# Kernel optimization log

Measured on AMD Instinct MI355X. Metric: run time of the kernel, lower is better.

Reference implementation:

```python
import jax, jax.numpy as jnp
import numpy as np

N_HEAD = 12

def setup_inputs() -> dict:
    key = jax.random.key(0)
    ks = jax.random.split(key, 5)
    B, T, C = 8, 1024, 768
    s = 0.02
    return {
        'x': jax.random.normal(ks[0], (B, T, C), dtype=jnp.float32),
        'w_attn': jax.random.normal(ks[1], (C, 3 * C), dtype=jnp.float32) * s,
        'b_attn': jax.random.normal(ks[2], (3 * C,), dtype=jnp.float32) * s,
        'w_proj': jax.random.normal(ks[3], (C, C), dtype=jnp.float32) * s,
        'b_proj': jax.random.normal(ks[4], (C,), dtype=jnp.float32) * s,
    }

def reference(x, w_attn, b_attn, w_proj, b_proj):
    B, T, C = x.shape
    H, D = N_HEAD, C // N_HEAD
    qkv = x @ w_attn + b_attn                      # [B,T,3C]
    q, k, v = jnp.split(qkv, 3, axis=-1)
    q = q.reshape(B, T, H, D)
    k = k.reshape(B, T, H, D)
    v = v.reshape(B, T, H, D)
    # NOTE: faithful to source - NO 1/sqrt(D) scaling
    wei = jnp.einsum('bthd,bshd->bhts', q, k)      # [B,H,T,T]
    causal = jnp.tril(jnp.ones((T, T), dtype=bool))
    wei = jnp.where(causal[None, None], wei, -jnp.inf)
    wei = jax.nn.softmax(wei, axis=-1)
    out = jnp.einsum('bhts,bshd->bthd', wei, v)    # [B,T,H,D]
    out = out.reshape(B, T, C)
    return out @ w_proj + b_proj
```

## Files before the change

kernel.cpp:

```cpp
#include <hip/hip_runtime.h>

typedef __attribute__((ext_vector_type(8))) short bf16x8_t;
typedef __attribute__((ext_vector_type(4))) float f32x4_t;

#define AS1C(p) ((const __attribute__((address_space(1))) void*)(p))
#define AS3(p)  ((__attribute__((address_space(3))) void*)(p))

#define N_HEAD 12
#define SEQ_T 1024
#define CDIM 768
#define HDIM 64
#define L2E 1.44269504f

__device__ __forceinline__ unsigned short f2bf(float f) {
    union { float f; unsigned int u; } v;
    v.f = f;
    unsigned int r = (v.u + 0x7fffu + ((v.u >> 16) & 1u)) >> 16;
    return (unsigned short)r;
}

__global__ __launch_bounds__(256) void prep(
    const float4* __restrict__ x4, ushort4* __restrict__ xbf4,
    const float* __restrict__ w_attn, unsigned short* __restrict__ waT,
    const float* __restrict__ w_proj, unsigned short* __restrict__ wpT)
{
    __shared__ float tile[32][33];
    const int blk = blockIdx.x;
    const int tid = threadIdx.x;
    if (blk < 6144) {
        int i = blk * 256 + tid;
        float4 v = x4[i];
        ushort4 o;
        o.x = f2bf(v.x); o.y = f2bf(v.y); o.z = f2bf(v.z); o.w = f2bf(v.w);
        xbf4[i] = o;
        return;
    }
    const float* src; unsigned short* dst; int R, Cc, c0, r0;
    if (blk < 7872) {
        int idx = blk - 6144;
        src = w_attn; dst = waT; R = 768; Cc = 2304;
        c0 = (idx % 72) * 32; r0 = (idx / 72) * 32;
    } else {
        int idx = blk - 7872;
        src = w_proj; dst = wpT; R = 768; Cc = 768;
        c0 = (idx % 24) * 32; r0 = (idx / 24) * 32;
    }
    const int tx = tid & 31, ty = tid >> 5;
#pragma unroll
    for (int i = 0; i < 4; i++)
        tile[ty + i * 8][tx] = src[(size_t)(r0 + ty + i * 8) * Cc + c0 + tx];
    __syncthreads();
#pragma unroll
    for (int i = 0; i < 4; i++)
        dst[(size_t)(c0 + ty + i * 8) * R + r0 + tx] = f2bf(tile[tx][ty + i * 8]);
}

__device__ __forceinline__ void gemm128_core(
    const unsigned short* __restrict__ A, const unsigned short* __restrict__ Bt,
    unsigned short* As, unsigned short* Bs, f32x4_t acc[4][4], int mBase, int nBase)
{
    const int tid  = threadIdx.x;
    const int lane = tid & 63;
    const int wv   = tid >> 6;
    const int quad = lane >> 4;
    const int l16  = lane & 15;
    const int wm   = (wv >> 1) * 64;
    const int wn   = (wv & 1) * 64;

    f32x4_t zero = {0.f, 0.f, 0.f, 0.f};
#pragma unroll
    for (int tm = 0; tm < 4; tm++)
#pragma unroll
        for (int tn = 0; tn < 4; tn++)
            acc[tm][tn] = zero;

    for (int kt = 0; kt < 768; kt += 64) {
#pragma unroll
        for (int i = 0; i < 4; i++) {
            int cbase = i * 256 + wv * 64;
            int ci = cbase + lane;
            int r = ci >> 3;
            int koff = (((ci & 7) ^ (r & 7)) << 3);
            __builtin_amdgcn_global_load_lds(
                AS1C(A + (size_t)(mBase + r) * 768 + kt + koff),
                AS3(As + cbase * 8), 16, 0, 0);
            __builtin_amdgcn_global_load_lds(
                AS1C(Bt + (size_t)(nBase + r) * 768 + kt + koff),
                AS3(Bs + cbase * 8), 16, 0, 0);
        }
        __syncthreads();
#pragma unroll
        for (int ks = 0; ks < 2; ks++) {
            bf16x8_t af[4], bfv[4];
#pragma unroll
            for (int tm = 0; tm < 4; tm++)
                af[tm] = *(const bf16x8_t*)(As + (wm + tm * 16 + l16) * 64 +
                                            (((ks * 4 + quad) ^ (l16 & 7)) << 3));
#pragma unroll
            for (int tn = 0; tn < 4; tn++)
                bfv[tn] = *(const bf16x8_t*)(Bs + (wn + tn * 16 + l16) * 64 +
                                             (((ks * 4 + quad) ^ (l16 & 7)) << 3));
#pragma unroll
            for (int tm = 0; tm < 4; tm++)
#pragma unroll
                for (int tn = 0; tn < 4; tn++)
                    acc[tm][tn] = __builtin_amdgcn_mfma_f32_16x16x32_bf16(
                        af[tm], bfv[tn], acc[tm][tn], 0, 0, 0);
        }
        __syncthreads();
    }
}

__global__ __launch_bounds__(256) void gemm_qkv(
    const unsigned short* __restrict__ x, const unsigned short* __restrict__ waT,
    const float* __restrict__ b_attn,
    unsigned short* __restrict__ qbuf, unsigned short* __restrict__ kbuf,
    unsigned short* __restrict__ vbuf)
{
    __shared__ __align__(16) unsigned short As[128 * 64];
    __shared__ __align__(16) unsigned short Bs[128 * 64];
    f32x4_t acc[4][4];
    const int lid = blockIdx.x;
    const int xcd = lid & 7;
    const int j = lid >> 3;
    const int mTile = xcd * 8 + (j & 7);
    const int nTile = j >> 3;
    const int mBase = mTile * 128;
    const int nBase = nTile * 128;
    gemm128_core(x, waT, As, Bs, acc, mBase, nBase);

    const int tid = threadIdx.x;
    const int lane = tid & 63, wv = tid >> 6;
    const int quad = lane >> 4, l16 = lane & 15;
    const int wm = (wv >> 1) * 64, wn = (wv & 1) * 64;
    const int part = nTile / 6;

#pragma unroll
    for (int tn = 0; tn < 4; tn++) {
        int n = nBase + wn + tn * 16 + l16;
        float bv = b_attn[n];
        int f = n - part * 768;
        int hh = f >> 6, d = f & 63;
        if (part == 2) {
#pragma unroll
            for (int tm = 0; tm < 4; tm++) {
                int t0 = mBase + wm + tm * 16 + quad * 4;
                int bb = t0 >> 10, tt = t0 & 1023;
                ushort4 pk;
                pk.x = f2bf(acc[tm][tn][0] + bv);
                pk.y = f2bf(acc[tm][tn][1] + bv);
                pk.z = f2bf(acc[tm][tn][2] + bv);
                pk.w = f2bf(acc[tm][tn][3] + bv);
                *(ushort4*)(vbuf + ((size_t)(bb * N_HEAD + hh) * HDIM + d) * SEQ_T + tt) = pk;
            }
        } else {
            const float scale = (part == 0) ? L2E : 1.f;
            unsigned short* dst = (part == 0) ? qbuf : kbuf;
#pragma unroll
            for (int tm = 0; tm < 4; tm++) {
#pragma unroll
                for (int i = 0; i < 4; i++) {
                    int row = mBase + wm + tm * 16 + quad * 4 + i;
                    int bb = row >> 10, tt = row & 1023;
                    dst[((size_t)(bb * N_HEAD + hh) * SEQ_T + tt) * HDIM + d] =
                        f2bf((acc[tm][tn][i] + bv) * scale);
                }
            }
        }
    }
}

__device__ __forceinline__ void mask_exp_pack(
    f32x4_t s[4], int diag, int qloc, int quad,
    float& lsum, unsigned int u[4][2])
{
    if (diag) {
#pragma unroll
        for (int c = 0; c < 4; c++)
#pragma unroll
            for (int i = 0; i < 4; i++)
                if (c * 16 + quad * 4 + i > qloc) s[c][i] = -1e30f;
    }
    float p[4][4];
#pragma unroll
    for (int c = 0; c < 4; c++)
#pragma unroll
        for (int i = 0; i < 4; i++)
            p[c][i] = exp2f(s[c][i]);
#pragma unroll
    for (int c = 0; c < 4; c++)
        lsum += (p[c][0] + p[c][1]) + (p[c][2] + p[c][3]);
#pragma unroll
    for (int c = 0; c < 4; c++)
#pragma unroll
        for (int i2 = 0; i2 < 2; i2++)
            u[c][i2] = (unsigned int)f2bf(p[c][2 * i2]) |
                       ((unsigned int)f2bf(p[c][2 * i2 + 1]) << 16);
}

__device__ __forceinline__ void p_write(
    unsigned short* pw, const unsigned int u[4][2], int quad, int l16)
{
#pragma unroll
    for (int c = 0; c < 4; c++)
#pragma unroll
        for (int i2 = 0; i2 < 2; i2++) {
            int g = c * 2 + (quad >> 1);
            *(unsigned int*)(pw + l16 * 64 + ((g ^ (l16 & 7)) << 3) +
                             4 * (quad & 1) + 2 * i2) = u[c][i2];
        }
}

__global__ __launch_bounds__(256, 3) void attn_fused(
    const unsigned short* __restrict__ qb, const unsigned short* __restrict__ kb,
    const unsigned short* __restrict__ vb, unsigned short* __restrict__ attb)
{
    __shared__ __align__(16) unsigned short Kbuf[2][64 * 64];
    __shared__ __align__(16) unsigned short Vbuf[2][64 * 64];
    __shared__ __align__(16) unsigned short Psh[4][16 * 64];

    const int bhx = blockIdx.x;
    const int t   = blockIdx.y;
    const int h = bhx % N_HEAD;
    const int b = bhx / N_HEAD;
    const int tid = threadIdx.x;
    const int lane = tid & 63, wv = tid >> 6;
    const int quad = lane >> 4, l16 = lane & 15;
    const int tB = 15 - t, kmax = 15 - t;
    const int qloc = wv * 16 + l16;

    const size_t bh = (size_t)(b * N_HEAD + h);
    const unsigned short* kbase = kb + bh * SEQ_T * HDIM;
    const unsigned short* vbase = vb + bh * HDIM * SEQ_T;
    const unsigned short* qpt   = qb + bh * SEQ_T * HDIM;

    const int j0 = wv * 128 + lane, j1 = j0 + 64;
    const int r0 = j0 >> 3, g0 = (j0 & 7) ^ (r0 & 7);
    const int r1 = j1 >> 3, g1 = (j1 & 7) ^ (r1 & 7);
    const int rgK0 = r0 * 64 + g0 * 8,   rgK1 = r1 * 64 + g1 * 8;
    const int rgV0 = r0 * 1024 + g0 * 8, rgV1 = r1 * 1024 + g1 * 8;
    const int ldsc0 = (wv * 128) * 8, ldsc1 = (wv * 128 + 64) * 8;

    bf16x8_t qfA[2], qfB[2];
    {
        const unsigned short* qa  = qpt + (size_t)(t * 64 + qloc) * HDIM;
        const unsigned short* qbp = qpt + (size_t)(tB * 64 + qloc) * HDIM;
#pragma unroll
        for (int kc = 0; kc < 2; kc++) {
            qfA[kc] = *(const bf16x8_t*)(qa + kc * 32 + quad * 8);
            qfB[kc] = *(const bf16x8_t*)(qbp + kc * 32 + quad * 8);
        }
    }

    f32x4_t zero = {0.f, 0.f, 0.f, 0.f};
    f32x4_t oA[4], oB[4];
#pragma unroll
    for (int c = 0; c < 4; c++) { oA[c] = zero; oB[c] = zero; }
    float lA = 0.f, lB = 0.f;

    __builtin_amdgcn_global_load_lds(AS1C(kbase + rgK0), AS3(&Kbuf[0][0] + ldsc0), 16, 0, 0);
    __builtin_amdgcn_global_load_lds(AS1C(kbase + rgK1), AS3(&Kbuf[0][0] + ldsc1), 16, 0, 0);
    __builtin_amdgcn_global_load_lds(AS1C(vbase + rgV0), AS3(&Vbuf[0][0] + ldsc0), 16, 0, 0);
    __builtin_amdgcn_global_load_lds(AS1C(vbase + rgV1), AS3(&Vbuf[0][0] + ldsc1), 16, 0, 0);
    __syncthreads();

    for (int kt = 0; kt <= kmax; kt++) {
        const int cur = kt & 1, nxt = cur ^ 1;
        if (kt < kmax) {
            const unsigned short* kp = kbase + (kt + 1) * 4096;
            const unsigned short* vp = vbase + (kt + 1) * 64;
            __builtin_amdgcn_global_load_lds(AS1C(kp + rgK0), AS3(&Kbuf[nxt][0] + ldsc0), 16, 0, 0);
            __builtin_amdgcn_global_load_lds(AS1C(kp + rgK1), AS3(&Kbuf[nxt][0] + ldsc1), 16, 0, 0);
            __builtin_amdgcn_global_load_lds(AS1C(vp + rgV0), AS3(&Vbuf[nxt][0] + ldsc0), 16, 0, 0);
            __builtin_amdgcn_global_load_lds(AS1C(vp + rgV1), AS3(&Vbuf[nxt][0] + ldsc1), 16, 0, 0);
        }

        const unsigned short* Kc = &Kbuf[cur][0];
        const unsigned short* Vc = &Vbuf[cur][0];
        const int doA = (kt <= t);

        bf16x8_t vf[4][2];
#pragma unroll
        for (int nc = 0; nc < 4; nc++)
#pragma unroll
            for (int kc = 0; kc < 2; kc++)
                vf[nc][kc] = *(const bf16x8_t*)(Vc + (nc * 16 + l16) * 64 +
                                                (((kc * 4 + quad) ^ (l16 & 7)) << 3));

        f32x4_t sB[4], sA[4];
#pragma unroll
        for (int c = 0; c < 4; c++) {
            bf16x8_t kf0 = *(const bf16x8_t*)(Kc + (c * 16 + l16) * 64 +
                                              ((quad ^ (l16 & 7)) << 3));
            bf16x8_t kf1 = *(const bf16x8_t*)(Kc + (c * 16 + l16) * 64 +
                                              (((4 + quad) ^ (l16 & 7)) << 3));
            sB[c] = __builtin_amdgcn_mfma_f32_16x16x32_bf16(kf0, qfB[0], zero, 0, 0, 0);
            sB[c] = __builtin_amdgcn_mfma_f32_16x16x32_bf16(kf1, qfB[1], sB[c], 0, 0, 0);
            if (doA) {
                sA[c] = __builtin_amdgcn_mfma_f32_16x16x32_bf16(kf0, qfA[0], zero, 0, 0, 0);
                sA[c] = __builtin_amdgcn_mfma_f32_16x16x32_bf16(kf1, qfA[1], sA[c], 0, 0, 0);
            }
        }

        unsigned short* pw = &Psh[wv][0];
        unsigned int uB[4][2], uA[4][2];

        mask_exp_pack(sB, kt == tB, qloc, quad, lB, uB);
        __asm__ __volatile__("" ::: "memory");
        p_write(pw, uB, quad, l16);
        if (doA)
            mask_exp_pack(sA, kt == t, qloc, quad, lA, uA);
        __asm__ __volatile__("" ::: "memory");
        bf16x8_t pfB[2];
#pragma unroll
        for (int kc = 0; kc < 2; kc++)
            pfB[kc] = *(const bf16x8_t*)(pw + l16 * 64 + (((kc * 4 + quad) ^ (l16 & 7)) << 3));
        __asm__ __volatile__("" ::: "memory");
#pragma unroll
        for (int kc = 0; kc < 2; kc++)
#pragma unroll
            for (int nc = 0; nc < 4; nc++)
                oB[nc] = __builtin_amdgcn_mfma_f32_16x16x32_bf16(pfB[kc], vf[nc][kc], oB[nc], 0, 0, 0);
        if (doA) {
            p_write(pw, uA, quad, l16);
            __asm__ __volatile__("" ::: "memory");
            bf16x8_t pfA[2];
#pragma unroll
            for (int kc = 0; kc < 2; kc++)
                pfA[kc] = *(const bf16x8_t*)(pw + l16 * 64 + (((kc * 4 + quad) ^ (l16 & 7)) << 3));
#pragma unroll
            for (int kc = 0; kc < 2; kc++)
#pragma unroll
                for (int nc = 0; nc < 4; nc++)
                    oA[nc] = __builtin_amdgcn_mfma_f32_16x16x32_bf16(pfA[kc], vf[nc][kc], oA[nc], 0, 0, 0);
        }
        __syncthreads();
    }

    lA += __shfl_xor(lA, 16); lA += __shfl_xor(lA, 32);
    lB += __shfl_xor(lB, 16); lB += __shfl_xor(lB, 32);
    float invA = 1.f / lA, invB = 1.f / lB;
    float iA[4], iB[4];
#pragma unroll
    for (int i = 0; i < 4; i++) {
        iA[i] = __shfl(invA, quad * 4 + i);
        iB[i] = __shfl(invB, quad * 4 + i);
    }

#pragma unroll
    for (int nc = 0; nc < 4; nc++)
#pragma unroll
        for (int i = 0; i < 4; i++) {
            int rowA = t * 64 + wv * 16 + quad * 4 + i;
            int rowB = tB * 64 + wv * 16 + quad * 4 + i;
            int col = h * HDIM + nc * 16 + l16;
            attb[((size_t)b * SEQ_T + rowA) * CDIM + col] = f2bf(oA[nc][i] * iA[i]);
            attb[((size_t)b * SEQ_T + rowB) * CDIM + col] = f2bf(oB[nc][i] * iB[i]);
        }
}

__global__ __launch_bounds__(256) void gemm_proj(
    const unsigned short* __restrict__ attb, const unsigned short* __restrict__ wpT,
    const float* __restrict__ b_proj, float* __restrict__ out)
{
    __shared__ __align__(16) unsigned short As[64 * 64];
    __shared__ __align__(16) unsigned short Bs[128 * 64];
    const int lid = blockIdx.x;
    const int xcd = lid & 7;
    const int j = lid >> 3;
    const int mTile = xcd * 16 + (j & 15);
    const int nTile = j >> 4;
    const int mBase = mTile * 64;
    const int nBase = nTile * 128;

    const int tid  = threadIdx.x;
    const int lane = tid & 63;
    const int wv   = tid >> 6;
    const int quad = lane >> 4;
    const int l16  = lane & 15;
    const int wm   = (wv >> 1) * 32;
    const int wn   = (wv & 1) * 64;

    f32x4_t zero = {0.f, 0.f, 0.f, 0.f};
    f32x4_t acc[2][4];
#pragma unroll
    for (int tm = 0; tm < 2; tm++)
#pragma unroll
        for (int tn = 0; tn < 4; tn++)
            acc[tm][tn] = zero;

    for (int kt = 0; kt < 768; kt += 64) {
#pragma unroll
        for (int i = 0; i < 2; i++) {
            int cbase = i * 256 + wv * 64;
            int ci = cbase + lane;
            int r = ci >> 3;
            int koff = (((ci & 7) ^ (r & 7)) << 3);
            __builtin_amdgcn_global_load_lds(
                AS1C(attb + (size_t)(mBase + r) * 768 + kt + koff),
                AS3(As + cbase * 8), 16, 0, 0);
        }
#pragma unroll
        for (int i = 0; i < 4; i++) {
            int cbase = i * 256 + wv * 64;
            int ci = cbase + lane;
            int r = ci >> 3;
            int koff = (((ci & 7) ^ (r & 7)) << 3);
            __builtin_amdgcn_global_load_lds(
                AS1C(wpT + (size_t)(nBase + r) * 768 + kt + koff),
                AS3(Bs + cbase * 8), 16, 0, 0);
        }
        __syncthreads();
#pragma unroll
        for (int ks = 0; ks < 2; ks++) {
            bf16x8_t af[2], bfv[4];
#pragma unroll
            for (int tm = 0; tm < 2; tm++)
                af[tm] = *(const bf16x8_t*)(As + (wm + tm * 16 + l16) * 64 +
                                            (((ks * 4 + quad) ^ (l16 & 7)) << 3));
#pragma unroll
            for (int tn = 0; tn < 4; tn++)
                bfv[tn] = *(const bf16x8_t*)(Bs + (wn + tn * 16 + l16) * 64 +
                                             (((ks * 4 + quad) ^ (l16 & 7)) << 3));
#pragma unroll
            for (int tm = 0; tm < 2; tm++)
#pragma unroll
                for (int tn = 0; tn < 4; tn++)
                    acc[tm][tn] = __builtin_amdgcn_mfma_f32_16x16x32_bf16(
                        af[tm], bfv[tn], acc[tm][tn], 0, 0, 0);
        }
        __syncthreads();
    }

#pragma unroll
    for (int tn = 0; tn < 4; tn++) {
        int n = nBase + wn + tn * 16 + l16;
        float bv = b_proj[n];
#pragma unroll
        for (int tm = 0; tm < 2; tm++)
#pragma unroll
            for (int i = 0; i < 4; i++) {
                int row = mBase + wm + tm * 16 + quad * 4 + i;
                out[(size_t)row * CDIM + n] = acc[tm][tn][i] + bv;
            }
    }
}

extern "C" void kernel_launch(void* const* d_in, const int* in_sizes, int n_in,
                              void* d_out, int out_size, void* d_ws, size_t ws_size,
                              hipStream_t stream) {
    const float* x      = (const float*)d_in[0];
    const float* w_attn = (const float*)d_in[1];
    const float* b_attn = (const float*)d_in[2];
    const float* w_proj = (const float*)d_in[3];
    const float* b_proj = (const float*)d_in[4];
    float* out = (float*)d_out;

    unsigned short* ws   = (unsigned short*)d_ws;
    unsigned short* waT  = ws;
    unsigned short* wpT  = waT + 1769472;
    unsigned short* xbf  = wpT + 589824;
    unsigned short* qbuf = xbf + 6291456;
    unsigned short* kbuf = qbuf + 6291456;
    unsigned short* vbuf = kbuf + 6291456;
    unsigned short* attb = vbuf + 6291456;

    prep<<<dim3(8448), 256, 0, stream>>>((const float4*)x, (ushort4*)xbf,
                                         w_attn, waT, w_proj, wpT);
    gemm_qkv<<<dim3(1152), 256, 0, stream>>>(xbf, waT, b_attn, qbuf, kbuf, vbuf);
    attn_fused<<<dim3(96, 8), 256, 0, stream>>>(qbuf, kbuf, vbuf, attb);
    gemm_proj<<<dim3(768), 256, 0, stream>>>(attb, wpT, b_proj, out);
}
```

Before: 186.0 us.

## Use triple-buffered 128x256 GEMM tiles with 8 waves for QKV and projection

Both GEMMs now share one core that uses 512 threads and 128x256 output tiles, with a three-stage LDS ring. The next two k-tiles are loaded by direct global-to-LDS copies while the current one is computed, gated by explicit vmcnt waits and raw barriers. This is meant to hide global load latency and raise data reuse per block. In exchange it uses far more LDS (about 147 KB per block) and much fewer blocks, only 192 for the projection, which may leave compute units underfilled.

```diff
diff --git a/kernel.cpp b/kernel.cpp
--- a/kernel.cpp
+++ b/kernel.cpp
@@ -55,17 +55,73 @@
         dst[(size_t)(c0 + ty + i * 8) * R + r0 + tx] = f2bf(tile[tx][ty + i * 8]);
 }
 
-__device__ __forceinline__ void gemm128_core(
+#define KTILES 12
+#define ASTRIDE (128 * 64)
+#define BSTRIDE (256 * 64)
+
+__device__ __forceinline__ void stage_tile(
     const unsigned short* __restrict__ A, const unsigned short* __restrict__ Bt,
-    unsigned short* As, unsigned short* Bs, f32x4_t acc[4][4], int mBase, int nBase)
+    unsigned short* As, unsigned short* Bs, int mBase, int nBase, int kt,
+    int wv, int lane)
+{
+#pragma unroll
+    for (int i = 0; i < 2; i++) {
+        int cbase = i * 512 + wv * 64;
+        int ci = cbase + lane;
+        int r = ci >> 3;
+        int koff = (((ci & 7) ^ (r & 7)) << 3);
+        __builtin_amdgcn_global_load_lds(
+            AS1C(A + (size_t)(mBase + r) * 768 + kt + koff),
+            AS3(As + cbase * 8), 16, 0, 0);
+    }
+#pragma unroll
+    for (int i = 0; i < 4; i++) {
+        int cbase = i * 512 + wv * 64;
+        int ci = cbase + lane;
+        int r = ci >> 3;
+        int koff = (((ci & 7) ^ (r & 7)) << 3);
+        __builtin_amdgcn_global_load_lds(
+            AS1C(Bt + (size_t)(nBase + r) * 768 + kt + koff),
+            AS3(Bs + cbase * 8), 16, 0, 0);
+    }
+}
+
+__device__ __forceinline__ void compute_tile(
+    const unsigned short* As, const unsigned short* Bs,
+    f32x4_t acc[4][4], int wm, int wn, int quad, int l16)
+{
+#pragma unroll
+    for (int ks = 0; ks < 2; ks++) {
+        bf16x8_t af[4], bfv[4];
+#pragma unroll
+        for (int tm = 0; tm < 4; tm++)
+            af[tm] = *(const bf16x8_t*)(As + (wm + tm * 16 + l16) * 64 +
+                                        (((ks * 4 + quad) ^ (l16 & 7)) << 3));
+#pragma unroll
+        for (int tn = 0; tn < 4; tn++)
+            bfv[tn] = *(const bf16x8_t*)(Bs + (wn + tn * 16 + l16) * 64 +
+                                         (((ks * 4 + quad) ^ (l16 & 7)) << 3));
+#pragma unroll
+        for (int tm = 0; tm < 4; tm++)
+#pragma unroll
+            for (int tn = 0; tn < 4; tn++)
+                acc[tm][tn] = __builtin_amdgcn_mfma_f32_16x16x32_bf16(
+                    af[tm], bfv[tn], acc[tm][tn], 0, 0, 0);
+    }
+}
+
+__device__ __forceinline__ void gemm_core8(
+    const unsigned short* __restrict__ A, const unsigned short* __restrict__ Bt,
+    unsigned short* As, unsigned short* Bs, f32x4_t acc[4][4],
+    int mBase, int nBase)
 {
     const int tid  = threadIdx.x;
     const int lane = tid & 63;
     const int wv   = tid >> 6;
     const int quad = lane >> 4;
     const int l16  = lane & 15;
-    const int wm   = (wv >> 1) * 64;
-    const int wn   = (wv & 1) * 64;
+    const int wm   = (wv >> 2) * 64;
+    const int wn   = (wv & 3) * 64;
 
     f32x4_t zero = {0.f, 0.f, 0.f, 0.f};
 #pragma unroll
@@ -74,51 +130,39 @@
         for (int tn = 0; tn < 4; tn++)
             acc[tm][tn] = zero;
 
-    for (int kt = 0; kt < 768; kt += 64) {
-#pragma unroll
-        for (int i = 0; i < 4; i++) {
-            int cbase = i * 256 + wv * 64;
-            int ci = cbase + lane;
-            int r = ci >> 3;
-            int koff = (((ci & 7) ^ (r & 7)) << 3);
-            __builtin_amdgcn_global_load_lds(
-                AS1C(A + (size_t)(mBase + r) * 768 + kt + koff),
-                AS3(As + cbase * 8), 16, 0, 0);
-            __builtin_amdgcn_global_load_lds(
-                AS1C(Bt + (size_t)(nBase + r) * 768 + kt + koff),
-                AS3(Bs + cbase * 8), 16, 0, 0);
-        }
-        __syncthreads();
-#pragma unroll
-        for (int ks = 0; ks < 2; ks++) {
-            bf16x8_t af[4], bfv[4];
-#pragma unroll
-            for (int tm = 0; tm < 4; tm++)
-                af[tm] = *(const bf16x8_t*)(As + (wm + tm * 16 + l16) * 64 +
-                                            (((ks * 4 + quad) ^ (l16 & 7)) << 3));
-#pragma unroll
-            for (int tn = 0; tn < 4; tn++)
-                bfv[tn] = *(const bf16x8_t*)(Bs + (wn + tn * 16 + l16) * 64 +
-                                             (((ks * 4 + quad) ^ (l16 & 7)) << 3));
-#pragma unroll
-            for (int tm = 0; tm < 4; tm++)
-#pragma unroll
-                for (int tn = 0; tn < 4; tn++)
-                    acc[tm][tn] = __builtin_amdgcn_mfma_f32_16x16x32_bf16(
-                        af[tm], bfv[tn], acc[tm][tn], 0, 0, 0);
-        }
-        __syncthreads();
-    }
-}
-
-__global__ __launch_bounds__(256) void gemm_qkv(
+    stage_tile(A, Bt, As + 0 * ASTRIDE, Bs + 0 * BSTRIDE, mBase, nBase, 0, wv, lane);
+    stage_tile(A, Bt, As + 1 * ASTRIDE, Bs + 1 * BSTRIDE, mBase, nBase, 64, wv, lane);
+
+#pragma unroll
+    for (int t = 0; t < KTILES; t++) {
+        if (t + 2 < KTILES) {
+            const int nb = (t + 2) % 3;
+            stage_tile(A, Bt, As + nb * ASTRIDE, Bs + nb * BSTRIDE,
+                       mBase, nBase, (t + 2) * 64, wv, lane);
+        }
+        if (t + 2 < KTILES)
+            asm volatile("s_waitcnt vmcnt(12)" ::: "memory");
+        else if (t + 1 < KTILES)
+            asm volatile("s_waitcnt vmcnt(6)" ::: "memory");
+        else
+            asm volatile("s_waitcnt vmcnt(0)" ::: "memory");
+        __builtin_amdgcn_s_barrier();
+        asm volatile("" ::: "memory");
+        const int cb = t % 3;
+        compute_tile(As + cb * ASTRIDE, Bs + cb * BSTRIDE, acc, wm, wn, quad, l16);
+        asm volatile("" ::: "memory");
+        __builtin_amdgcn_s_barrier();
+    }
+}
+
+__global__ __launch_bounds__(512) void gemm_qkv(
     const unsigned short* __restrict__ x, const unsigned short* __restrict__ waT,
     const float* __restrict__ b_attn,
     unsigned short* __restrict__ qbuf, unsigned short* __restrict__ kbuf,
     unsigned short* __restrict__ vbuf)
 {
-    __shared__ __align__(16) unsigned short As[128 * 64];
-    __shared__ __align__(16) unsigned short Bs[128 * 64];
+    __shared__ __align__(16) unsigned short As[3 * ASTRIDE];
+    __shared__ __align__(16) unsigned short Bs[3 * BSTRIDE];
     f32x4_t acc[4][4];
     const int lid = blockIdx.x;
     const int xcd = lid & 7;
@@ -126,14 +170,14 @@
     const int mTile = xcd * 8 + (j & 7);
     const int nTile = j >> 3;
     const int mBase = mTile * 128;
-    const int nBase = nTile * 128;
-    gemm128_core(x, waT, As, Bs, acc, mBase, nBase);
+    const int nBase = nTile * 256;
+    gemm_core8(x, waT, As, Bs, acc, mBase, nBase);
 
     const int tid = threadIdx.x;
     const int lane = tid & 63, wv = tid >> 6;
     const int quad = lane >> 4, l16 = lane & 15;
-    const int wm = (wv >> 1) * 64, wn = (wv & 1) * 64;
-    const int part = nTile / 6;
+    const int wm = (wv >> 2) * 64, wn = (wv & 3) * 64;
+    const int part = nTile / 3;
 
 #pragma unroll
     for (int tn = 0; tn < 4; tn++) {
@@ -359,85 +403,36 @@
         }
 }
 
-__global__ __launch_bounds__(256) void gemm_proj(
+__global__ __launch_bounds__(512) void gemm_proj(
     const unsigned short* __restrict__ attb, const unsigned short* __restrict__ wpT,
     const float* __restrict__ b_proj, float* __restrict__ out)
 {
-    __shared__ __align__(16) unsigned short As[64 * 64];
-    __shared__ __align__(16) unsigned short Bs[128 * 64];
+    __shared__ __align__(16) unsigned short As[3 * ASTRIDE];
+    __shared__ __align__(16) unsigned short Bs[3 * BSTRIDE];
+    f32x4_t acc[4][4];
     const int lid = blockIdx.x;
     const int xcd = lid & 7;
     const int j = lid >> 3;
-    const int mTile = xcd * 16 + (j & 15);
-    const int nTile = j >> 4;
-    const int mBase = mTile * 64;
-    const int nBase = nTile * 128;
+    const int mTile = xcd * 8 + (j & 7);
+    const int nTile = j >> 3;
+    const int mBase = mTile * 128;
+    const int nBase = nTile * 256;
+    gemm_core8(attb, wpT, As, Bs, acc, mBase, nBase);
 
     const int tid  = threadIdx.x;
     const int lane = tid & 63;
     const int wv   = tid >> 6;
     const int quad = lane >> 4;
     const int l16  = lane & 15;
-    const int wm   = (wv >> 1) * 32;
-    const int wn   = (wv & 1) * 64;
-
-    f32x4_t zero = {0.f, 0.f, 0.f, 0.f};
-    f32x4_t acc[2][4];
-#pragma unroll
-    for (int tm = 0; tm < 2; tm++)
-#pragma unroll
-        for (int tn = 0; tn < 4; tn++)
-            acc[tm][tn] = zero;
-
-    for (int kt = 0; kt < 768; kt += 64) {
-#pragma unroll
-        for (int i = 0; i < 2; i++) {
-            int cbase = i * 256 + wv * 64;
-            int ci = cbase + lane;
-            int r = ci >> 3;
-            int koff = (((ci & 7) ^ (r & 7)) << 3);
-            __builtin_amdgcn_global_load_lds(
-                AS1C(attb + (size_t)(mBase + r) * 768 + kt + koff),
-                AS3(As + cbase * 8), 16, 0, 0);
-        }
-#pragma unroll
-        for (int i = 0; i < 4; i++) {
-            int cbase = i * 256 + wv * 64;
-            int ci = cbase + lane;
-            int r = ci >> 3;
-            int koff = (((ci & 7) ^ (r & 7)) << 3);
-            __builtin_amdgcn_global_load_lds(
-                AS1C(wpT + (size_t)(nBase + r) * 768 + kt + koff),
-                AS3(Bs + cbase * 8), 16, 0, 0);
-        }
-        __syncthreads();
-#pragma unroll
-        for (int ks = 0; ks < 2; ks++) {
-            bf16x8_t af[2], bfv[4];
-#pragma unroll
-            for (int tm = 0; tm < 2; tm++)
-                af[tm] = *(const bf16x8_t*)(As + (wm + tm * 16 + l16) * 64 +
-                                            (((ks * 4 + quad) ^ (l16 & 7)) << 3));
-#pragma unroll
-            for (int tn = 0; tn < 4; tn++)
-                bfv[tn] = *(const bf16x8_t*)(Bs + (wn + tn * 16 + l16) * 64 +
-                                             (((ks * 4 + quad) ^ (l16 & 7)) << 3));
-#pragma unroll
-            for (int tm = 0; tm < 2; tm++)
-#pragma unroll
-                for (int tn = 0; tn < 4; tn++)
-                    acc[tm][tn] = __builtin_amdgcn_mfma_f32_16x16x32_bf16(
-                        af[tm], bfv[tn], acc[tm][tn], 0, 0, 0);
-        }
-        __syncthreads();
-    }
+    const int wm   = (wv >> 2) * 64;
+    const int wn   = (wv & 3) * 64;
 
 #pragma unroll
     for (int tn = 0; tn < 4; tn++) {
         int n = nBase + wn + tn * 16 + l16;
         float bv = b_proj[n];
 #pragma unroll
-        for (int tm = 0; tm < 2; tm++)
+        for (int tm = 0; tm < 4; tm++)
 #pragma unroll
             for (int i = 0; i < 4; i++) {
                 int row = mBase + wm + tm * 16 + quad * 4 + i;
@@ -467,7 +462,7 @@
 
     prep<<<dim3(8448), 256, 0, stream>>>((const float4*)x, (ushort4*)xbf,
                                          w_attn, waT, w_proj, wpT);
-    gemm_qkv<<<dim3(1152), 256, 0, stream>>>(xbf, waT, b_attn, qbuf, kbuf, vbuf);
+    gemm_qkv<<<dim3(576), 512, 0, stream>>>(xbf, waT, b_attn, qbuf, kbuf, vbuf);
     attn_fused<<<dim3(96, 8), 256, 0, stream>>>(qbuf, kbuf, vbuf, attb);
-    gemm_proj<<<dim3(768), 256, 0, stream>>>(attb, wpT, b_proj, out);
-}
+    gemm_proj<<<dim3(192), 512, 0, stream>>>(attb, wpT, b_proj, out);
+}
```

New measurement: 182.3 us. 2.0% less time.

## Double-buffer LDS tiles in QKV and projection GEMMs to overlap loads with MFMA

Applied to the files above, without the earlier changes.

Both GEMM kernels now use two LDS buffers per operand and issue the global-to-LDS loads for the next K tile before computing on the current one. The goal is to hide global load latency behind the MFMA work instead of stalling on a barrier every K step. The cost is doubled LDS use per block (64KB for the QKV GEMM), which may reduce occupancy. Correctness also depends on the one remaining barrier per iteration covering completion of the async LDS loads.

```diff
diff --git a/kernel.cpp b/kernel.cpp
--- a/kernel.cpp
+++ b/kernel.cpp
@@ -55,9 +55,30 @@
         dst[(size_t)(c0 + ty + i * 8) * R + r0 + tx] = f2bf(tile[tx][ty + i * 8]);
 }
 
+__device__ __forceinline__ void stage128(
+    const unsigned short* __restrict__ A, const unsigned short* __restrict__ Bt,
+    unsigned short* As, unsigned short* Bs, int mBase, int nBase, int kt,
+    int wv, int lane)
+{
+#pragma unroll
+    for (int i = 0; i < 4; i++) {
+        int cbase = i * 256 + wv * 64;
+        int ci = cbase + lane;
+        int r = ci >> 3;
+        int koff = (((ci & 7) ^ (r & 7)) << 3);
+        __builtin_amdgcn_global_load_lds(
+            AS1C(A + (size_t)(mBase + r) * 768 + kt + koff),
+            AS3(As + cbase * 8), 16, 0, 0);
+        __builtin_amdgcn_global_load_lds(
+            AS1C(Bt + (size_t)(nBase + r) * 768 + kt + koff),
+            AS3(Bs + cbase * 8), 16, 0, 0);
+    }
+}
+
 __device__ __forceinline__ void gemm128_core(
     const unsigned short* __restrict__ A, const unsigned short* __restrict__ Bt,
-    unsigned short* As, unsigned short* Bs, f32x4_t acc[4][4], int mBase, int nBase)
+    unsigned short (*As)[128 * 64], unsigned short (*Bs)[128 * 64],
+    f32x4_t acc[4][4], int mBase, int nBase)
 {
     const int tid  = threadIdx.x;
     const int lane = tid & 63;
@@ -74,31 +95,27 @@
         for (int tn = 0; tn < 4; tn++)
             acc[tm][tn] = zero;
 
-    for (int kt = 0; kt < 768; kt += 64) {
-#pragma unroll
-        for (int i = 0; i < 4; i++) {
-            int cbase = i * 256 + wv * 64;
-            int ci = cbase + lane;
-            int r = ci >> 3;
-            int koff = (((ci & 7) ^ (r & 7)) << 3);
-            __builtin_amdgcn_global_load_lds(
-                AS1C(A + (size_t)(mBase + r) * 768 + kt + koff),
-                AS3(As + cbase * 8), 16, 0, 0);
-            __builtin_amdgcn_global_load_lds(
-                AS1C(Bt + (size_t)(nBase + r) * 768 + kt + koff),
-                AS3(Bs + cbase * 8), 16, 0, 0);
-        }
-        __syncthreads();
+    stage128(A, Bt, As[0], Bs[0], mBase, nBase, 0, wv, lane);
+    __syncthreads();
+
+    for (int kt = 0; kt < 12; kt++) {
+        const int cur = kt & 1;
+        if (kt < 11)
+            stage128(A, Bt, As[cur ^ 1], Bs[cur ^ 1], mBase, nBase,
+                     (kt + 1) * 64, wv, lane);
+        __asm__ __volatile__("" ::: "memory");
+        const unsigned short* Ac = As[cur];
+        const unsigned short* Bc = Bs[cur];
 #pragma unroll
         for (int ks = 0; ks < 2; ks++) {
             bf16x8_t af[4], bfv[4];
 #pragma unroll
             for (int tm = 0; tm < 4; tm++)
-                af[tm] = *(const bf16x8_t*)(As + (wm + tm * 16 + l16) * 64 +
+                af[tm] = *(const bf16x8_t*)(Ac + (wm + tm * 16 + l16) * 64 +
                                             (((ks * 4 + quad) ^ (l16 & 7)) << 3));
 #pragma unroll
             for (int tn = 0; tn < 4; tn++)
-                bfv[tn] = *(const bf16x8_t*)(Bs + (wn + tn * 16 + l16) * 64 +
+                bfv[tn] = *(const bf16x8_t*)(Bc + (wn + tn * 16 + l16) * 64 +
                                              (((ks * 4 + quad) ^ (l16 & 7)) << 3));
 #pragma unroll
             for (int tm = 0; tm < 4; tm++)
@@ -117,8 +134,8 @@
     unsigned short* __restrict__ qbuf, unsigned short* __restrict__ kbuf,
     unsigned short* __restrict__ vbuf)
 {
-    __shared__ __align__(16) unsigned short As[128 * 64];
-    __shared__ __align__(16) unsigned short Bs[128 * 64];
+    __shared__ __align__(16) unsigned short As[2][128 * 64];
+    __shared__ __align__(16) unsigned short Bs[2][128 * 64];
     f32x4_t acc[4][4];
     const int lid = blockIdx.x;
     const int xcd = lid & 7;
@@ -363,8 +380,8 @@
     const unsigned short* __restrict__ attb, const unsigned short* __restrict__ wpT,
     const float* __restrict__ b_proj, float* __restrict__ out)
 {
-    __shared__ __align__(16) unsigned short As[64 * 64];
-    __shared__ __align__(16) unsigned short Bs[128 * 64];
+    __shared__ __align__(16) unsigned short As[2][64 * 64];
+    __shared__ __align__(16) unsigned short Bs[2][128 * 64];
     const int lid = blockIdx.x;
     const int xcd = lid & 7;
     const int j = lid >> 3;
@@ -389,38 +406,50 @@
         for (int tn = 0; tn < 4; tn++)
             acc[tm][tn] = zero;
 
-    for (int kt = 0; kt < 768; kt += 64) {
-#pragma unroll
-        for (int i = 0; i < 2; i++) {
-            int cbase = i * 256 + wv * 64;
-            int ci = cbase + lane;
-            int r = ci >> 3;
-            int koff = (((ci & 7) ^ (r & 7)) << 3);
-            __builtin_amdgcn_global_load_lds(
-                AS1C(attb + (size_t)(mBase + r) * 768 + kt + koff),
-                AS3(As + cbase * 8), 16, 0, 0);
-        }
-#pragma unroll
-        for (int i = 0; i < 4; i++) {
-            int cbase = i * 256 + wv * 64;
-            int ci = cbase + lane;
-            int r = ci >> 3;
-            int koff = (((ci & 7) ^ (r & 7)) << 3);
-            __builtin_amdgcn_global_load_lds(
-                AS1C(wpT + (size_t)(nBase + r) * 768 + kt + koff),
-                AS3(Bs + cbase * 8), 16, 0, 0);
-        }
-        __syncthreads();
+#define PROJ_STAGE(buf, kt)                                                    \
+    {                                                                          \
+        _Pragma("unroll")                                                      \
+        for (int i = 0; i < 2; i++) {                  \
+            int cbase = i * 256 + wv * 64;                                     \
+            int ci = cbase + lane;                                             \
+            int r = ci >> 3;                                                   \
+            int koff = (((ci & 7) ^ (r & 7)) << 3);                            \
+            __builtin_amdgcn_global_load_lds(                                  \
+                AS1C(attb + (size_t)(mBase + r) * 768 + (kt) + koff),          \
+                AS3(As[buf] + cbase * 8), 16, 0, 0);                           \
+        }                                                                      \
+        _Pragma("unroll")                                                      \
+        for (int i = 0; i < 4; i++) {                 \
+            int cbase = i * 256 + wv * 64;                                     \
+            int ci = cbase + lane;                                             \
+            int r = ci >> 3;                                                   \
+            int koff = (((ci & 7) ^ (r & 7)) << 3);                            \
+            __builtin_amdgcn_global_load_lds(                                  \
+                AS1C(wpT + (size_t)(nBase + r) * 768 + (kt) + koff),           \
+                AS3(Bs[buf] + cbase * 8), 16, 0, 0);                           \
+        }                                                                      \
+    }
+
+    PROJ_STAGE(0, 0);
+    __syncthreads();
+
+    for (int kt = 0; kt < 12; kt++) {
+        const int cur = kt & 1;
+        if (kt < 11)
+            PROJ_STAGE(cur ^ 1, (kt + 1) * 64);
+        __asm__ __volatile__("" ::: "memory");
+        const unsigned short* Ac = As[cur];
+        const unsigned short* Bc = Bs[cur];
 #pragma unroll
         for (int ks = 0; ks < 2; ks++) {
             bf16x8_t af[2], bfv[4];
 #pragma unroll
             for (int tm = 0; tm < 2; tm++)
-                af[tm] = *(const bf16x8_t*)(As + (wm + tm * 16 + l16) * 64 +
+                af[tm] = *(const bf16x8_t*)(Ac + (wm + tm * 16 + l16) * 64 +
                                             (((ks * 4 + quad) ^ (l16 & 7)) << 3));
 #pragma unroll
             for (int tn = 0; tn < 4; tn++)
-                bfv[tn] = *(const bf16x8_t*)(Bs + (wn + tn * 16 + l16) * 64 +
+                bfv[tn] = *(const bf16x8_t*)(Bc + (wn + tn * 16 + l16) * 64 +
                                              (((ks * 4 + quad) ^ (l16 & 7)) << 3));
 #pragma unroll
             for (int tm = 0; tm < 2; tm++)
@@ -431,6 +460,7 @@
         }
         __syncthreads();
     }
+#undef PROJ_STAGE
 
 #pragma unroll
     for (int tn = 0; tn < 4; tn++) {
```

New measurement: 185.9 us. No clear change (-0.1%).
